# Kernel tuning notes

Hardware: AMD Instinct MI355X
Metric: run time of the kernel (lower is better)

Reference implementation:

```python
import jax, jax.numpy as jnp
import numpy as np

MARGIN = 1.0
EPS = 1e-12


def setup_inputs() -> dict:
    key = jax.random.key(0)
    k1, k2, k3 = jax.random.split(key, 3)
    B, C, D = 16384, 500, 512
    features = jax.random.normal(k1, (B, D), dtype=jnp.float32)
    prototypes = jax.random.normal(k2, (C, D), dtype=jnp.float32)
    labels = jax.random.randint(k3, (B,), 0, C, dtype=jnp.int64)
    return {"features": features, "prototypes": prototypes, "labels": labels}


def reference(features, prototypes, labels):
    # Pairwise L2 distances [B, C] via the expanded form (no [B,C,D] intermediate)
    f2 = jnp.sum(features * features, axis=-1, keepdims=True)   # [B, 1]
    p2 = jnp.sum(prototypes * prototypes, axis=-1)               # [C]
    sq = f2 + p2 - 2.0 * (features @ prototypes.T)               # [B, C]
    dists = jnp.sqrt(jnp.maximum(sq, EPS))                       # [B, C]

    B, C = dists.shape
    d_pos = jnp.take_along_axis(dists, labels[:, None], axis=1)[:, 0]  # [B]
    pos_mask = jax.nn.one_hot(labels, C, dtype=bool)             # [B, C]
    d_neg_min = jnp.min(jnp.where(pos_mask, jnp.inf, dists), axis=-1)  # [B]

    loss = jnp.mean(jax.nn.relu(d_pos - d_neg_min + MARGIN))
    return loss
```

## Files before the change

kernel.cpp:

```cpp
#include <hip/hip_runtime.h>
#include <stdint.h>
#include <stddef.h>

#define BB 16384
#define CC 500
#define DD 512
#define PADC 512
#define LMARGIN 1.0f
#define EPSQ 1e-12f
#define NK 16

typedef __attribute__((ext_vector_type(8))) _Float16 f16x8;
typedef __attribute__((ext_vector_type(4))) _Float16 f16x4;
typedef __attribute__((ext_vector_type(4))) float f32x4;

#define GLOBAL_AS __attribute__((address_space(1)))
#define LDS_AS __attribute__((address_space(3)))

__device__ __forceinline__ void ld_lds16(const void* g, void* l) {
  __builtin_amdgcn_global_load_lds((const GLOBAL_AS void*)g, (LDS_AS void*)l, 16, 0, 0);
}

__global__ void prepP_kernel(const float* __restrict__ protos,
                             unsigned short* __restrict__ protoH,
                             float* __restrict__ p2,
                             float* __restrict__ out) {
  int c = blockIdx.x * 4 + (threadIdx.x >> 6);
  int lane = threadIdx.x & 63;
  if (c == 0 && lane == 0) out[0] = 0.f;
  f32x4 a0 = {0.f, 0.f, 0.f, 0.f}, a1 = a0;
  if (c < CC) {
    const float* src = protos + (size_t)c * DD + lane * 8;
    a0 = *(const f32x4*)src;
    a1 = *(const f32x4*)(src + 4);
  }
  f16x8 h;
  float s = 0.f;
#pragma unroll
  for (int u = 0; u < 4; ++u) {
    h[u] = (_Float16)a0[u];
    h[u + 4] = (_Float16)a1[u];
    s = fmaf(a0[u], a0[u], s);
    s = fmaf(a1[u], a1[u], s);
  }
  *(f16x8*)(protoH + (size_t)c * DD + lane * 8) = h;
#pragma unroll
  for (int d = 1; d < 64; d <<= 1) s += __shfl_xor(s, d, 64);
  if (lane == 0) p2[c] = s;
}

__launch_bounds__(512, 2)
__global__ void main_kernel(const float* __restrict__ feat,
                            const unsigned short* __restrict__ protoH,
                            const float* __restrict__ p2,
                            const int* __restrict__ labels,
                            float* __restrict__ out) {
  __shared__ __align__(16) unsigned short Bb[2][PADC * 32];
  __shared__ __align__(16) unsigned short Ab[2][64 * 32];
  __shared__ float p2l[PADC];
  __shared__ float f2l[64];
  __shared__ int labl[64];
  __shared__ float redM[4][64], redP[4][64];

  const int tid = threadIdx.x;
  const int w = tid >> 6;
  const int lane = tid & 63;
  const int lane16 = lane & 15;
  const int quad = lane >> 4;
  const int mh = w & 1;
  const int nq = w >> 1;
  const int r0 = blockIdx.x * 64;

  const int arow = tid >> 3;
  const int akoff = (tid & 7) * 4;
  const float* aSrc = feat + (size_t)(r0 + arow) * DD + akoff;

  const char* pB = (const char*)protoH;
  const char* bSrc[4];
  int bDst[4];
#pragma unroll
  for (int j = 0; j < 4; ++j) {
    int col = (w * 4 + j) * 16 + (lane >> 2);
    bSrc[j] = pB + (size_t)col * (DD * 2) + (lane & 3) * 16;
    bDst[j] = (w * 4 + j) * 1024 + lane * 16;
  }

#pragma unroll
  for (int j = 0; j < 4; ++j) ld_lds16(bSrc[j], (char*)&Bb[0][0] + bDst[j]);

  float f2acc = 0.f;
  {
    f32x4 a = *(const f32x4*)aSrc;
    f16x4 h;
#pragma unroll
    for (int u = 0; u < 4; ++u) {
      h[u] = (_Float16)a[u];
      f2acc = fmaf(a[u], a[u], f2acc);
    }
    *(f16x4*)(&Ab[0][arow * 32 + akoff]) = h;
  }
  p2l[tid] = p2[tid];
  if (tid < 64) labl[tid] = labels[r0 + tid];

  f32x4 acc[2][8];
#pragma unroll
  for (int ms = 0; ms < 2; ++ms)
#pragma unroll
    for (int ns = 0; ns < 8; ++ns) acc[ms][ns] = (f32x4){0.f, 0.f, 0.f, 0.f};

  __syncthreads();

  int buf = 0;
  for (int kc = 0; kc < NK; ++kc) {
    f32x4 aNext;
    if (kc + 1 < NK) {
#pragma unroll
      for (int j = 0; j < 4; ++j)
        ld_lds16(bSrc[j] + (kc + 1) * 64, (char*)&Bb[buf ^ 1][0] + bDst[j]);
      aNext = *(const f32x4*)(aSrc + (kc + 1) * 32);
    }

    f16x8 af[2], bfr[8];
#pragma unroll
    for (int ms = 0; ms < 2; ++ms)
      af[ms] = *(const f16x8*)(&Ab[buf][(mh * 32 + ms * 16 + lane16) * 32 +
                                        quad * 8]);
#pragma unroll
    for (int ns = 0; ns < 8; ++ns)
      bfr[ns] = *(const f16x8*)(&Bb[buf][(nq * 128 + ns * 16 + lane16) * 32 +
                                         quad * 8]);
#pragma unroll
    for (int ms = 0; ms < 2; ++ms)
#pragma unroll
      for (int ns = 0; ns < 8; ++ns)
        acc[ms][ns] = __builtin_amdgcn_mfma_f32_16x16x32_f16(
            af[ms], bfr[ns], acc[ms][ns], 0, 0, 0);

    if (kc + 1 < NK) {
      f16x4 h;
#pragma unroll
      for (int u = 0; u < 4; ++u) {
        h[u] = (_Float16)aNext[u];
        f2acc = fmaf(aNext[u], aNext[u], f2acc);
      }
      *(f16x4*)(&Ab[buf ^ 1][arow * 32 + akoff]) = h;
    }

    __syncthreads();
    buf ^= 1;
  }

  f2acc += __shfl_xor(f2acc, 1, 64);
  f2acc += __shfl_xor(f2acc, 2, 64);
  f2acc += __shfl_xor(f2acc, 4, 64);
  if ((tid & 7) == 0) f2l[arow] = f2acc;
  __syncthreads();

#pragma unroll
  for (int ms = 0; ms < 2; ++ms) {
#pragma unroll
    for (int i = 0; i < 4; ++i) {
      const int rowIn = mh * 32 + ms * 16 + quad * 4 + i;
      const float f2v = f2l[rowIn];
      const int lb = labl[rowIn];
      float m = 1e30f, p = -1e30f;
#pragma unroll
      for (int ns = 0; ns < 8; ++ns) {
        const int col = nq * 128 + ns * 16 + lane16;
        float d = sqrtf(fmaxf(f2v + p2l[col] - 2.f * acc[ms][ns][i], EPSQ));
        bool isPos = (col == lb);
        p = fmaxf(p, isPos ? d : -1e30f);
        m = fminf(m, (!isPos && col < CC) ? d : 1e30f);
      }
#pragma unroll
      for (int d = 1; d < 16; d <<= 1) {
        m = fminf(m, __shfl_xor(m, d, 64));
        p = fmaxf(p, __shfl_xor(p, d, 64));
      }
      if (lane16 == 0) {
        redM[nq][rowIn] = m;
        redP[nq][rowIn] = p;
      }
    }
  }
  __syncthreads();

  if (tid < 64) {
    float m = fminf(fminf(redM[0][tid], redM[1][tid]),
                    fminf(redM[2][tid], redM[3][tid]));
    float p = fmaxf(fmaxf(redP[0][tid], redP[1][tid]),
                    fmaxf(redP[2][tid], redP[3][tid]));
    float term = fmaxf(p - m + LMARGIN, 0.f);
#pragma unroll
    for (int d = 1; d < 64; d <<= 1) term += __shfl_xor(term, d, 64);
    if (tid == 0) atomicAdd(out, term * (1.0f / BB));
  }
}

extern "C" void kernel_launch(void* const* d_in, const int* in_sizes, int n_in,
                              void* d_out, int out_size, void* d_ws, size_t ws_size,
                              hipStream_t stream) {
  const float* feat = (const float*)d_in[0];
  const float* protos = (const float*)d_in[1];
  const int* labels = (const int*)d_in[2];
  float* out = (float*)d_out;

  char* ws = (char*)d_ws;
  unsigned short* protoH = (unsigned short*)(ws);
  float* p2 = (float*)(ws + (1 << 20));

  prepP_kernel<<<PADC / 4, 256, 0, stream>>>(protos, protoH, p2, out);
  main_kernel<<<BB / 64, 512, 0, stream>>>(feat, protoH, p2, labels, out);
}
```

Baseline: 99.75 us.

## Restructure GEMM: stage full A tile in LDS, stream B from global into registers

The main kernel now loads and converts the block's entire 64x512 feature tile into LDS once. Each wave streams its own 64 prototype columns directly from global memory into registers with a one-step prefetch, which removes the per-k-step LDS double buffering and the __syncthreads inside the loop. The epilogue also defers the sqrt: it reduces on p2-2*dot and writes per-wave partial min/max to a workspace. A new third kernel then adds f2, takes the sqrt and computes the loss. The trade-off is an extra launch and workspace traffic, plus B fragments read from global/L2 without any LDS sharing.

```diff
diff --git a/kernel.cpp b/kernel.cpp
--- a/kernel.cpp
+++ b/kernel.cpp
@@ -13,13 +13,6 @@
 typedef __attribute__((ext_vector_type(8))) _Float16 f16x8;
 typedef __attribute__((ext_vector_type(4))) _Float16 f16x4;
 typedef __attribute__((ext_vector_type(4))) float f32x4;
-
-#define GLOBAL_AS __attribute__((address_space(1)))
-#define LDS_AS __attribute__((address_space(3)))
-
-__device__ __forceinline__ void ld_lds16(const void* g, void* l) {
-  __builtin_amdgcn_global_load_lds((const GLOBAL_AS void*)g, (LDS_AS void*)l, 16, 0, 0);
-}
 
 __global__ void prepP_kernel(const float* __restrict__ protos,
                              unsigned short* __restrict__ protoH,
@@ -54,147 +47,133 @@
                             const unsigned short* __restrict__ protoH,
                             const float* __restrict__ p2,
                             const int* __restrict__ labels,
-                            float* __restrict__ out) {
-  __shared__ __align__(16) unsigned short Bb[2][PADC * 32];
-  __shared__ __align__(16) unsigned short Ab[2][64 * 32];
-  __shared__ float p2l[PADC];
-  __shared__ float f2l[64];
-  __shared__ int labl[64];
-  __shared__ float redM[4][64], redP[4][64];
+                            float* __restrict__ f2ws,
+                            float2* __restrict__ ws2) {
+  __shared__ __align__(16) unsigned short Afull[NK][64][32];
 
   const int tid = threadIdx.x;
   const int w = tid >> 6;
   const int lane = tid & 63;
   const int lane16 = lane & 15;
   const int quad = lane >> 4;
-  const int mh = w & 1;
-  const int nq = w >> 1;
   const int r0 = blockIdx.x * 64;
 
-  const int arow = tid >> 3;
-  const int akoff = (tid & 7) * 4;
-  const float* aSrc = feat + (size_t)(r0 + arow) * DD + akoff;
+  const unsigned short* pb = protoH + (size_t)(w * 64 + lane16) * DD + quad * 8;
 
-  const char* pB = (const char*)protoH;
-  const char* bSrc[4];
-  int bDst[4];
+  f16x8 bcur[4], bnxt[4];
 #pragma unroll
-  for (int j = 0; j < 4; ++j) {
-    int col = (w * 4 + j) * 16 + (lane >> 2);
-    bSrc[j] = pB + (size_t)col * (DD * 2) + (lane & 3) * 16;
-    bDst[j] = (w * 4 + j) * 1024 + lane * 16;
+  for (int nt = 0; nt < 4; ++nt) bcur[nt] = *(const f16x8*)(pb + nt * 16 * DD);
+
+  {
+    const f32x4* fsrc = (const f32x4*)(feat + (size_t)r0 * DD);
+    f32x4 a[NK];
+#pragma unroll
+    for (int i = 0; i < NK; ++i) a[i] = fsrc[w * 1024 + i * 64 + lane];
+
+    float f2row[8] = {0.f, 0.f, 0.f, 0.f, 0.f, 0.f, 0.f, 0.f};
+#pragma unroll
+    for (int i = 0; i < NK; ++i) {
+      const int row = w * 8 + (i >> 1);
+      const int k = (i & 1) * 256 + lane * 4;
+      f16x4 h;
+      float s = 0.f;
+#pragma unroll
+      for (int u = 0; u < 4; ++u) {
+        h[u] = (_Float16)a[i][u];
+        s = fmaf(a[i][u], a[i][u], s);
+      }
+      *(f16x4*)(&Afull[k >> 5][row][k & 31]) = h;
+#pragma unroll
+      for (int d = 1; d < 64; d <<= 1) s += __shfl_xor(s, d, 64);
+      f2row[i >> 1] += s;
+    }
+    if (lane == 0) {
+#pragma unroll
+      for (int j = 0; j < 8; ++j) f2ws[r0 + w * 8 + j] = f2row[j];
+    }
   }
 
+  f32x4 acc[4][4];
 #pragma unroll
-  for (int j = 0; j < 4; ++j) ld_lds16(bSrc[j], (char*)&Bb[0][0] + bDst[j]);
-
-  float f2acc = 0.f;
-  {
-    f32x4 a = *(const f32x4*)aSrc;
-    f16x4 h;
+  for (int mt = 0; mt < 4; ++mt)
 #pragma unroll
-    for (int u = 0; u < 4; ++u) {
-      h[u] = (_Float16)a[u];
-      f2acc = fmaf(a[u], a[u], f2acc);
-    }
-    *(f16x4*)(&Ab[0][arow * 32 + akoff]) = h;
-  }
-  p2l[tid] = p2[tid];
-  if (tid < 64) labl[tid] = labels[r0 + tid];
-
-  f32x4 acc[2][8];
-#pragma unroll
-  for (int ms = 0; ms < 2; ++ms)
-#pragma unroll
-    for (int ns = 0; ns < 8; ++ns) acc[ms][ns] = (f32x4){0.f, 0.f, 0.f, 0.f};
+    for (int nt = 0; nt < 4; ++nt) acc[mt][nt] = (f32x4){0.f, 0.f, 0.f, 0.f};
 
   __syncthreads();
 
-  int buf = 0;
+#pragma unroll 2
   for (int kc = 0; kc < NK; ++kc) {
-    f32x4 aNext;
     if (kc + 1 < NK) {
 #pragma unroll
-      for (int j = 0; j < 4; ++j)
-        ld_lds16(bSrc[j] + (kc + 1) * 64, (char*)&Bb[buf ^ 1][0] + bDst[j]);
-      aNext = *(const f32x4*)(aSrc + (kc + 1) * 32);
+      for (int nt = 0; nt < 4; ++nt)
+        bnxt[nt] = *(const f16x8*)(pb + nt * 16 * DD + (kc + 1) * 32);
     }
-
-    f16x8 af[2], bfr[8];
+    f16x8 af[4];
 #pragma unroll
-    for (int ms = 0; ms < 2; ++ms)
-      af[ms] = *(const f16x8*)(&Ab[buf][(mh * 32 + ms * 16 + lane16) * 32 +
-                                        quad * 8]);
+    for (int mt = 0; mt < 4; ++mt)
+      af[mt] = *(const f16x8*)(&Afull[kc][mt * 16 + lane16][0] + quad * 8);
 #pragma unroll
-    for (int ns = 0; ns < 8; ++ns)
-      bfr[ns] = *(const f16x8*)(&Bb[buf][(nq * 128 + ns * 16 + lane16) * 32 +
-                                         quad * 8]);
+    for (int mt = 0; mt < 4; ++mt)
 #pragma unroll
-    for (int ms = 0; ms < 2; ++ms)
+      for (int nt = 0; nt < 4; ++nt)
+        acc[mt][nt] = __builtin_amdgcn_mfma_f32_16x16x32_f16(
+            af[mt], bcur[nt], acc[mt][nt], 0, 0, 0);
 #pragma unroll
-      for (int ns = 0; ns < 8; ++ns)
-        acc[ms][ns] = __builtin_amdgcn_mfma_f32_16x16x32_f16(
-            af[ms], bfr[ns], acc[ms][ns], 0, 0, 0);
-
-    if (kc + 1 < NK) {
-      f16x4 h;
-#pragma unroll
-      for (int u = 0; u < 4; ++u) {
-        h[u] = (_Float16)aNext[u];
-        f2acc = fmaf(aNext[u], aNext[u], f2acc);
-      }
-      *(f16x4*)(&Ab[buf ^ 1][arow * 32 + akoff]) = h;
-    }
-
-    __syncthreads();
-    buf ^= 1;
+    for (int nt = 0; nt < 4; ++nt) bcur[nt] = bnxt[nt];
   }
 
-  f2acc += __shfl_xor(f2acc, 1, 64);
-  f2acc += __shfl_xor(f2acc, 2, 64);
-  f2acc += __shfl_xor(f2acc, 4, 64);
-  if ((tid & 7) == 0) f2l[arow] = f2acc;
-  __syncthreads();
+  float p2v[4];
+#pragma unroll
+  for (int nt = 0; nt < 4; ++nt) p2v[nt] = p2[w * 64 + nt * 16 + lane16];
 
 #pragma unroll
-  for (int ms = 0; ms < 2; ++ms) {
+  for (int mt = 0; mt < 4; ++mt) {
 #pragma unroll
     for (int i = 0; i < 4; ++i) {
-      const int rowIn = mh * 32 + ms * 16 + quad * 4 + i;
-      const float f2v = f2l[rowIn];
-      const int lb = labl[rowIn];
-      float m = 1e30f, p = -1e30f;
+      const int row = mt * 16 + quad * 4 + i;
+      const int lb = labels[r0 + row];
+      float qm = 1e30f, qp = -1e30f;
 #pragma unroll
-      for (int ns = 0; ns < 8; ++ns) {
-        const int col = nq * 128 + ns * 16 + lane16;
-        float d = sqrtf(fmaxf(f2v + p2l[col] - 2.f * acc[ms][ns][i], EPSQ));
+      for (int nt = 0; nt < 4; ++nt) {
+        const int col = w * 64 + nt * 16 + lane16;
+        float q = p2v[nt] - 2.f * acc[mt][nt][i];
         bool isPos = (col == lb);
-        p = fmaxf(p, isPos ? d : -1e30f);
-        m = fminf(m, (!isPos && col < CC) ? d : 1e30f);
+        qp = fmaxf(qp, isPos ? q : -1e30f);
+        qm = fminf(qm, (!isPos && col < CC) ? q : 1e30f);
       }
 #pragma unroll
       for (int d = 1; d < 16; d <<= 1) {
-        m = fminf(m, __shfl_xor(m, d, 64));
-        p = fmaxf(p, __shfl_xor(p, d, 64));
+        qm = fminf(qm, __shfl_xor(qm, d, 64));
+        qp = fmaxf(qp, __shfl_xor(qp, d, 64));
       }
-      if (lane16 == 0) {
-        redM[nq][rowIn] = m;
-        redP[nq][rowIn] = p;
-      }
+      if (lane16 == 0) ws2[(size_t)(r0 + row) * 8 + w] = make_float2(qm, qp);
     }
   }
+}
+
+__global__ void reduce_kernel(const float2* __restrict__ ws2,
+                              const float* __restrict__ f2ws,
+                              float* __restrict__ out) {
+  int row = blockIdx.x * 256 + threadIdx.x;
+  const float4* v = (const float4*)ws2;
+  float qm = 1e30f, qp = -1e30f;
+#pragma unroll
+  for (int j = 0; j < 4; ++j) {
+    float4 a = v[(size_t)row * 4 + j];
+    qm = fminf(qm, fminf(a.x, a.z));
+    qp = fmaxf(qp, fmaxf(a.y, a.w));
+  }
+  float f2 = f2ws[row];
+  float dn = sqrtf(fmaxf(f2 + qm, EPSQ));
+  float dp = sqrtf(fmaxf(f2 + qp, EPSQ));
+  float term = fmaxf(dp - dn + LMARGIN, 0.f);
+#pragma unroll
+  for (int d = 1; d < 64; d <<= 1) term += __shfl_xor(term, d, 64);
+  __shared__ float ws4[4];
+  if ((threadIdx.x & 63) == 0) ws4[threadIdx.x >> 6] = term;
   __syncthreads();
-
-  if (tid < 64) {
-    float m = fminf(fminf(redM[0][tid], redM[1][tid]),
-                    fminf(redM[2][tid], redM[3][tid]));
-    float p = fmaxf(fmaxf(redP[0][tid], redP[1][tid]),
-                    fmaxf(redP[2][tid], redP[3][tid]));
-    float term = fmaxf(p - m + LMARGIN, 0.f);
-#pragma unroll
-    for (int d = 1; d < 64; d <<= 1) term += __shfl_xor(term, d, 64);
-    if (tid == 0) atomicAdd(out, term * (1.0f / BB));
-  }
+  if (threadIdx.x == 0)
+    atomicAdd(out, (ws4[0] + ws4[1] + ws4[2] + ws4[3]) * (1.0f / BB));
 }
 
 extern "C" void kernel_launch(void* const* d_in, const int* in_sizes, int n_in,
@@ -207,8 +186,11 @@
 
   char* ws = (char*)d_ws;
   unsigned short* protoH = (unsigned short*)(ws);
-  float* p2 = (float*)(ws + (1 << 20));
+  float* p2 = (float*)(ws + (512 << 10));
+  float* f2ws = (float*)(ws + (1 << 20));
+  float2* ws2 = (float2*)(ws + (2 << 20));
 
   prepP_kernel<<<PADC / 4, 256, 0, stream>>>(protos, protoH, p2, out);
-  main_kernel<<<BB / 64, 512, 0, stream>>>(feat, protoH, p2, labels, out);
+  main_kernel<<<BB / 64, 512, 0, stream>>>(feat, protoH, p2, labels, f2ws, ws2);
+  reduce_kernel<<<BB / 256, 256, 0, stream>>>(ws2, f2ws, out);
 }
```

New measurement: 101.7 us. About the same (+2.0%).
